# Optimization experiments

Measured on AMD Instinct MI355X. Metric: run time of the kernel, lower is better.

Reference implementation:

```python
import jax, jax.numpy as jnp
import numpy as np

B, L, E = 4, 2048, 768
H, MLP = 12, 3072
DH = E // H
N_HASHES, QC, KC = 4, 128, 128
EPS = 1e-6


def _layernorm(x, g, b):
    m = jnp.mean(x, -1, keepdims=True)
    v = jnp.mean((x - m) ** 2, -1, keepdims=True)
    return (x - m) * jax.lax.rsqrt(v + EPS) * g + b


def _smyrf_attn(q, k, v, alpha, beta):
    # q, k, v: (bs, L, dh) with bs = B*H; q is pre-scaled by dh**-0.5
    bs, sl, dh = q.shape
    # ---- LSH clustering (no-grad region, matches torch.no_grad in SMYRF) ----
    qd = jax.lax.stop_gradient(q)
    kd = jax.lax.stop_gradient(k)
    q_sq = jnp.sum(qd * qd, -1, keepdims=True)
    k_sq = jnp.sum(kd * kd, -1, keepdims=True)
    m_tot = jnp.max(q_sq) + jnp.max(k_sq)  # XBOX+ max-norm constant
    zq = jnp.zeros_like(q_sq)
    Qx = jnp.concatenate([qd, jnp.sqrt(jnp.maximum(m_tot - q_sq, 0.0)), zq], -1)
    Kx = jnp.concatenate([kd, zq, jnp.sqrt(jnp.maximum(m_tot - k_sq, 0.0))], -1)
    # E2LSH: scalar projection per hash round; sort positions by hash value
    q_pos = jnp.argsort(jnp.transpose(Qx @ alpha + beta, (2, 0, 1)), -1)  # (nh, bs, L)
    k_pos = jnp.argsort(jnp.transpose(Kx @ alpha + beta, (2, 0, 1)), -1)

    def gather(x, pos):  # (bs,L,d), (nh,bs,L) -> (nh,bs,L,d)
        xb = jnp.broadcast_to(x[None], (N_HASHES,) + x.shape)
        return jnp.take_along_axis(xb, pos[..., None], axis=2)

    s_q = gather(q, q_pos).reshape(N_HASHES, bs, sl // QC, QC, dh)
    s_k = gather(k, k_pos).reshape(N_HASHES, bs, sl // KC, KC, dh)
    s_v = gather(v, k_pos).reshape(N_HASHES, bs, sl // KC, KC, dh)

    # within-cluster attention
    inner = jnp.einsum('hbnqd,hbnkd->hbnqk', s_q, s_k)
    lse = jax.nn.logsumexp(inner, axis=-1, keepdims=True)
    bo = jnp.einsum('hbnqk,hbnkd->hbnqd', jnp.exp(inner - lse), s_v)
    bo = bo.reshape(N_HASHES, bs, sl, dh)

    # undo the sort, merge hash rounds weighted by softmax denominators
    q_rev = jnp.argsort(q_pos, -1)  # (nh, bs, L)
    o = jnp.take_along_axis(bo, q_rev[..., None], axis=2)
    logits = jnp.take_along_axis(lse.reshape(N_HASHES, bs, sl), q_rev, axis=2)
    probs = jnp.exp(logits - jax.nn.logsumexp(logits, axis=0, keepdims=True))
    return jnp.sum(o * probs[..., None], axis=0)  # (bs, L, dh)


def reference(x, ln1_g, ln1_b, w_qkv, b_qkv, w_out, b_out, ln2_g, ln2_b,
              w1, b1, w2, b2, alpha, beta):
    h = _layernorm(x, ln1_g, ln1_b)
    qkv = h @ w_qkv.T + b_qkv  # (B, L, 3E)
    q, k, v = jnp.split(qkv, 3, axis=-1)
    to_heads = lambda t: t.reshape(B, L, H, DH).transpose(0, 2, 1, 3).reshape(B * H, L, DH)
    attn = _smyrf_attn(to_heads(q) * (DH ** -0.5), to_heads(k), to_heads(v), alpha, beta)
    attn = attn.reshape(B, H, L, DH).transpose(0, 2, 1, 3).reshape(B, L, E)
    x2 = x + attn @ w_out.T + b_out  # residual (dropout is identity at rate 0)
    y = _layernorm(x2, ln2_g, ln2_b)
    y = jax.nn.gelu(y @ w1.T + b1, approximate=False) @ w2.T + b2
    return x2 + y


def setup_inputs() -> dict:
    key = jax.random.key(0)
    ks = jax.random.split(key, 8)
    s = 0.02
    return {
        'x': jax.random.normal(ks[0], (B, L, E), jnp.float32),
        'ln1_g': jnp.ones((E,), jnp.float32),
        'ln1_b': jnp.zeros((E,), jnp.float32),
        'w_qkv': jax.random.normal(ks[1], (3 * E, E), jnp.float32) * s,
        'b_qkv': jnp.zeros((3 * E,), jnp.float32),
        'w_out': jax.random.normal(ks[2], (E, E), jnp.float32) * s,
        'b_out': jnp.zeros((E,), jnp.float32),
        'ln2_g': jnp.ones((E,), jnp.float32),
        'ln2_b': jnp.zeros((E,), jnp.float32),
        'w1': jax.random.normal(ks[3], (MLP, E), jnp.float32) * s,
        'b1': jnp.zeros((MLP,), jnp.float32),
        'w2': jax.random.normal(ks[4], (E, MLP), jnp.float32) * s,
        'b2': jnp.zeros((E,), jnp.float32),
        'alpha': jax.random.normal(ks[5], (DH + 2, N_HASHES), jnp.float32),
        'beta': jax.random.uniform(ks[6], (N_HASHES,), jnp.float32),
    }
```

## Files before the change

### kernel.cpp

```cpp
#include <hip/hip_runtime.h>
#include <hip/hip_bf16.h>

#define NB 4
#define SL 2048
#define EM 768
#define NHD 12
#define DHD 64
#define MLPD 3072
#define NHASH 4
#define NBS 48
#define NPOS 98304
#define MLROWS 8192

typedef __attribute__((ext_vector_type(8))) short short8;
typedef __attribute__((ext_vector_type(8))) _Float16 f16x8;
typedef __attribute__((ext_vector_type(4))) float f32x4;

__device__ __forceinline__ unsigned short f2bf(float x){
  unsigned u = __float_as_uint(x);
  u += 0x7fffu + ((u>>16)&1u);
  return (unsigned short)(u>>16);
}
__device__ __forceinline__ float bf2f(unsigned short s){
  return __uint_as_float(((unsigned)s)<<16);
}
__device__ __forceinline__ int sw128(int row, int colbyte){ return row*128 + (colbyte ^ ((row&7)<<4)); }
__device__ __forceinline__ int sw256(int row, int colbyte){ return row*256 + (colbyte ^ ((row&7)<<4)); }
__device__ __forceinline__ int sw64(int row, int slot){ return row*64 + ((slot ^ ((row>>1)&3))<<4); }

__device__ __forceinline__ void gll16(const void* g, const void* l){
  __builtin_amdgcn_global_load_lds(
      (const __attribute__((address_space(1))) void*)(uintptr_t)g,
      (__attribute__((address_space(3))) void*)(unsigned int)(uintptr_t)l,
      16, 0, 0);
}

__global__ __launch_bounds__(256) void prep_all(const float* __restrict__ wqkv,
    const float* __restrict__ wout, const float* __restrict__ w1, const float* __restrict__ w2,
    const float* __restrict__ bqkv, const float* __restrict__ alpha,
    const float* __restrict__ x, const float* __restrict__ ln1g, const float* __restrict__ ln1b,
    _Float16* __restrict__ wq_h, _Float16* __restrict__ wq_l,
    unsigned short* __restrict__ wo_b, unsigned short* __restrict__ w1_b, unsigned short* __restrict__ w2_b,
    _Float16* __restrict__ wh_h, _Float16* __restrict__ wh_l, float* __restrict__ bias_h,
    _Float16* __restrict__ hh, _Float16* __restrict__ hl){
  int bid = blockIdx.x, tid = threadIdx.x;
  if (bid < 27648){
    int i = bid*256 + tid;
    if (i < 1769472){
      float v = wqkv[i]*1024.0f;
      _Float16 h = (_Float16)v;
      wq_h[i] = h;
      wq_l[i] = (_Float16)((v - (float)h)*2048.0f);
    } else if (i < 2359296){
      int j = i - 1769472; wo_b[j] = f2bf(wout[j]);
    } else if (i < 4718592){
      int j = i - 2359296; w1_b[j] = f2bf(w1[j]);
    } else {
      int j = i - 4718592; w2_b[j] = f2bf(w2[j]);
    }
    return;
  }
  if (bid < 27776){
    int row = bid - 27648;
    if (row >= 96){
      for (int c = tid; c < 768; c += 256){ wh_h[row*768+c] = (_Float16)0.f; wh_l[row*768+c] = (_Float16)0.f; }
      if (tid==0) bias_h[row] = 0.f;
      return;
    }
    int qk = row/48, hh2 = (row%48)>>2, r = row&3;
    float s = qk ? 1.0f : 0.125f;
    int base = qk*768 + hh2*64;
    for (int c = tid; c < 768; c += 256){
      float acc = 0.f;
      #pragma unroll 8
      for (int d=0; d<64; d++)
        acc += wqkv[(size_t)(base+d)*768 + c] * alpha[d*4 + r];
      float v = acc*s*1024.0f;
      _Float16 h = (_Float16)v;
      wh_h[row*768+c] = h;
      wh_l[row*768+c] = (_Float16)((v - (float)h)*2048.0f);
    }
    if (tid==0){
      float b = 0.f;
      for (int d=0; d<64; d++) b += bqkv[base+d]*alpha[d*4+r];
      bias_h[row] = b*s;
    }
    return;
  }
  int row = bid - 27776;
  __shared__ float sb[8];
  const float* xr = x + (size_t)row*EM;
  float v0 = xr[tid], v1 = xr[tid+256], v2 = xr[tid+512];
  float s = v0+v1+v2;
  #pragma unroll
  for (int off=32; off; off>>=1) s += __shfl_down(s, off);
  if ((tid&63)==0) sb[tid>>6] = s;
  __syncthreads();
  float mean = (sb[0]+sb[1]+sb[2]+sb[3]) * (1.0f/768.0f);
  float d0=v0-mean, d1=v1-mean, d2=v2-mean;
  float q_ = d0*d0 + d1*d1 + d2*d2;
  #pragma unroll
  for (int off=32; off; off>>=1) q_ += __shfl_down(q_, off);
  __syncthreads();
  if ((tid&63)==0) sb[tid>>6] = q_;
  __syncthreads();
  float var = (sb[0]+sb[1]+sb[2]+sb[3]) * (1.0f/768.0f);
  float rs = rsqrtf(var + 1e-6f);
  float dv[3] = {d0,d1,d2};
  #pragma unroll
  for (int e=0;e<3;e++){
    int cc = tid + e*256;
    float val = dv[e]*rs*ln1g[cc] + ln1b[cc];
    size_t oi = (size_t)row*EM + cc;
    _Float16 h = (_Float16)val;
    hh[oi] = h;
    hl[oi] = (_Float16)((val - (float)h)*2048.0f);
  }
}

__global__ __launch_bounds__(256) void ln2_kernel(const unsigned short* __restrict__ xb,
    const float* __restrict__ g, const float* __restrict__ bb, unsigned short* __restrict__ ob){
  int row = blockIdx.x; int tid = threadIdx.x;
  __shared__ float sb[8];
  float v[4] = {0.f,0.f,0.f,0.f};
  const bool act = tid < 192;
  if (act){
    uint2 u = *(const uint2*)(xb + (size_t)row*EM + tid*4);
    v[0]=bf2f((unsigned short)(u.x&0xFFFF)); v[1]=bf2f((unsigned short)(u.x>>16));
    v[2]=bf2f((unsigned short)(u.y&0xFFFF)); v[3]=bf2f((unsigned short)(u.y>>16));
  }
  float s = v[0]+v[1]+v[2]+v[3];
  #pragma unroll
  for (int off=32; off; off>>=1) s += __shfl_down(s, off);
  if ((tid&63)==0) sb[tid>>6] = s;
  __syncthreads();
  float mean = (sb[0]+sb[1]+sb[2]+sb[3]) * (1.0f/768.0f);
  float d[4], q_ = 0.f;
  #pragma unroll
  for (int e=0;e<4;e++){ d[e] = act ? v[e]-mean : 0.f; q_ += d[e]*d[e]; }
  #pragma unroll
  for (int off=32; off; off>>=1) q_ += __shfl_down(q_, off);
  __syncthreads();
  if ((tid&63)==0) sb[tid>>6] = q_;
  __syncthreads();
  float var = (sb[0]+sb[1]+sb[2]+sb[3]) * (1.0f/768.0f);
  float rs = rsqrtf(var + 1e-6f);
  if (act){
    unsigned short o[4];
    #pragma unroll
    for (int e=0;e<4;e++){
      int cc = tid*4+e;
      o[e] = f2bf(d[e]*rs*g[cc] + bb[cc]);
    }
    uint2 u; u.x = (unsigned)o[0] | ((unsigned)o[1]<<16); u.y = (unsigned)o[2] | ((unsigned)o[3]<<16);
    *(uint2*)(ob + (size_t)row*EM + tid*4) = u;
  }
}

__global__ __launch_bounds__(512) void qkv_gemm(const _Float16* __restrict__ Ah, const _Float16* __restrict__ Al,
    const _Float16* __restrict__ Wh, const _Float16* __restrict__ Wl,
    const _Float16* __restrict__ wh_h, const _Float16* __restrict__ wh_l,
    const float* __restrict__ bias, const float* __restrict__ bias_h,
    unsigned short* __restrict__ qb16, unsigned short* __restrict__ kb16, unsigned short* __restrict__ vo,
    float* __restrict__ qsq, float* __restrict__ ksq, unsigned* __restrict__ scal,
    float* __restrict__ hqp, float* __restrict__ hkp){
  __shared__ __align__(16) char smem[65536];
  __shared__ float smx_s[8];
  const int tid=threadIdx.x, l=tid&63, w=tid>>6, wm=w>>1, wn=w&1;
  const int by = blockIdx.y;
  const int m0 = blockIdx.x*128;
  const int srow = l>>2;
  const int scol = ((l&3)^((l>>3)&3))<<3;
  int oa[2], ob_[4];
  #pragma unroll
  for (int i=0;i<2;i++) oa[i]  = sw64(wm*32 + i*16 + (l&15), l>>4);
  #pragma unroll
  for (int j=0;j<4;j++) ob_[j] = sw64(wn*64 + j*16 + (l&15), l>>4);
  const bool ishash = (by == 18);
  if (by < 12 || ishash){
    const int n0 = ishash ? 0 : by*128;
    const _Float16* Bh0 = ishash ? wh_h : (Wh + (size_t)n0*EM);
    const _Float16* Bl0 = ishash ? wh_l : (Wl + (size_t)n0*EM);
    const _Float16* pAh = Ah  + (size_t)(m0 + w*16 + srow)*EM + scol;
    const _Float16* pAl = Al  + (size_t)(m0 + w*16 + srow)*EM + scol;
    const _Float16* pBh = Bh0 + (size_t)(w*16 + srow)*EM + scol;
    const _Float16* pBl = Bl0 + (size_t)(w*16 + srow)*EM + scol;
    f32x4 a1[2][4] = {}; f32x4 a2[2][4] = {};
    auto stage = [&](int buf, int k0){
      char* b = smem + buf*32768 + w*1024;
      gll16(pAh + k0, b);
      gll16(pAl + k0, b +  8192);
      gll16(pBh + k0, b + 16384);
      gll16(pBl + k0, b + 24576);
    };
    auto compute = [&](int buf){
      char* s0 = smem + buf*32768;
      f16x8 ah[2], al2[2];
      #pragma unroll
      for (int i=0;i<2;i++){
        ah[i]  = *(const f16x8*)(s0 + oa[i]);
        al2[i] = *(const f16x8*)(s0 + 8192 + oa[i]);
      }
      #pragma unroll
      for (int j=0;j<4;j++){
        f16x8 bh = *(const f16x8*)(s0 + 16384 + ob_[j]);
        f16x8 bl = *(const f16x8*)(s0 + 24576 + ob_[j]);
        #pragma unroll
        for (int i=0;i<2;i++){
          a1[i][j] = __builtin_amdgcn_mfma_f32_16x16x32_f16(ah[i],  bh, a1[i][j],0,0,0);
          a2[i][j] = __builtin_amdgcn_mfma_f32_16x16x32_f16(ah[i],  bl, a2[i][j],0,0,0);
          a2[i][j] = __builtin_amdgcn_mfma_f32_16x16x32_f16(al2[i], bh, a2[i][j],0,0,0);
        }
      }
    };
    stage(0, 0);
    __syncthreads();
    #pragma unroll 2
    for (int t=0;t<24;t++){
      if (t<23) stage((t+1)&1, (t+1)*32);
      compute(t&1);
      __syncthreads();
    }
    if (ishash){
      #pragma unroll
      for (int i=0;i<2;i++)
      #pragma unroll
      for (int rr=0;rr<4;rr++){
        int gm = m0 + wm*32 + i*16 + (l>>4)*4 + rr;
        int b = gm>>11, ll = gm&2047;
        #pragma unroll
        for (int j=0;j<4;j++){
          int col = wn*64 + j*16 + (l&15);
          if (col < 96){
            float v = (a1[i][j][rr] + a2[i][j][rr]*4.8828125e-4f)*9.765625e-4f + bias_h[col];
            int qk = col/48, hh = (col%48)>>2, r = col&3;
            size_t pos = ((size_t)(b*NHD+hh))*SL + ll;
            (qk ? hkp : hqp)[(size_t)r*NPOS + pos] = v;
          }
        }
      }
    } else {
      const bool isq = (by < 6);
      const float so = isq ? 0.125f : 1.0f;
      unsigned short* ob16 = isq ? qb16 : kb16;
      float* sqout = isq ? qsq : ksq;
      const int gn0 = n0 + wn*64;
      const int hh = (isq ? gn0 : gn0-768)>>6;
      float mx = 0.f;
      #pragma unroll
      for (int i=0;i<2;i++)
      #pragma unroll
      for (int rr=0;rr<4;rr++){
        int gm = m0 + wm*32 + i*16 + (l>>4)*4 + rr;
        int b = gm>>11, ll = gm&2047;
        size_t pos = ((size_t)(b*NHD+hh))*SL + ll;
        float vv[4]; float sq_p = 0.f;
        #pragma unroll
        for (int j=0;j<4;j++){
          int gn = gn0 + j*16 + (l&15);
          float v = (a1[i][j][rr] + a2[i][j][rr]*4.8828125e-4f)*9.765625e-4f + bias[gn];
          v *= so;
          vv[j] = v;
          sq_p += v*v;
        }
        #pragma unroll
        for (int j=0;j<4;j++)
          ob16[pos*DHD + j*16 + (l&15)] = f2bf(vv[j]);
        #pragma unroll
        for (int off2=1; off2<16; off2<<=1) sq_p += __shfl_xor(sq_p, off2);
        mx = fmaxf(mx, sq_p);
        if ((l&15)==0) sqout[pos] = sq_p;
      }
      mx = fmaxf(mx, __shfl_xor(mx, 16));
      mx = fmaxf(mx, __shfl_xor(mx, 32));
      if (l==0) smx_s[w] = mx;
      __syncthreads();
      if (tid==0){
        float m2 = smx_s[0];
        #pragma unroll
        for (int q2=1;q2<8;q2++) m2 = fmaxf(m2, smx_s[q2]);
        atomicMax(scal + (isq?0:1), __float_as_uint(m2));
      }
    }
  } else {
    const int n0 = (by-12)*128;
    const _Float16* pAh = Ah + (size_t)(m0 + w*16 + srow)*EM + scol;
    const _Float16* pBh = Wh + (size_t)(1536 + n0 + w*16 + srow)*EM + scol;
    f32x4 acc[2][4] = {};
    auto stage = [&](int buf, int k0){
      char* b = smem + buf*16384 + w*1024;
      gll16(pAh + k0, b);
      gll16(pBh + k0, b + 8192);
    };
    auto compute = [&](int buf){
      char* s0 = smem + buf*16384;
      f16x8 ah[2];
      #pragma unroll
      for (int i=0;i<2;i++) ah[i] = *(const f16x8*)(s0 + oa[i]);
      #pragma unroll
      for (int j=0;j<4;j++){
        f16x8 bh = *(const f16x8*)(s0 + 8192 + ob_[j]);
        #pragma unroll
        for (int i=0;i<2;i++)
          acc[i][j] = __builtin_amdgcn_mfma_f32_16x16x32_f16(ah[i], bh, acc[i][j],0,0,0);
      }
    };
    stage(0, 0);
    __syncthreads();
    #pragma unroll 2
    for (int t=0;t<24;t++){
      if (t<23) stage((t+1)&1, (t+1)*32);
      compute(t&1);
      __syncthreads();
    }
    #pragma unroll
    for (int i=0;i<2;i++)
    #pragma unroll
    for (int j=0;j<4;j++)
    #pragma unroll
    for (int rr=0;rr<4;rr++){
      int gm = m0 + wm*32 + i*16 + (l>>4)*4 + rr;
      int gn = n0 + wn*64 + j*16 + (l&15);
      float v = acc[i][j][rr]*9.765625e-4f + bias[1536+gn];
      int hh = gn>>6; int d = gn&63;
      int b = gm>>11; int ll = gm&2047;
      vo[(((size_t)(b*NHD+hh))*SL + ll)*DHD + d] = f2bf(v);
    }
  }
}

__global__ __launch_bounds__(1024) void sort_kernel(const float* __restrict__ hqp, const float* __restrict__ hkp,
    const float* __restrict__ qsq, const float* __restrict__ ksq, const unsigned* __restrict__ scal,
    const float* __restrict__ alpha, const float* __restrict__ beta,
    int* __restrict__ qpos, int* __restrict__ kpos){
  __shared__ unsigned long long sv[2048];
  int bid = blockIdx.x;
  bool isq = bid < 192;
  int row = isq ? bid : bid-192;
  int r = row/NBS, bs = row%NBS;
  const float* hp  = (isq?hqp:hkp) + (size_t)r*NPOS + (size_t)bs*SL;
  const float* sqp = (isq?qsq:ksq) + (size_t)bs*SL;
  int* op = (isq?qpos:kpos) + (size_t)row*SL;
  float m_tot = __uint_as_float(scal[0]) + __uint_as_float(scal[1]);
  float ae = alpha[(isq?64:65)*4 + r];
  float be = beta[r];
  const int wv = threadIdx.x>>6, lane = threadIdx.x&63, seg = wv*128;
  #pragma unroll
  for (int s=0; s<2; s++){
    int i = seg + s*64 + lane;
    float ext = sqrtf(fmaxf(m_tot - sqp[i], 0.f));
    float h = hp[i] + ext*ae + be;
    unsigned u = __float_as_uint(h);
    u ^= ((unsigned)((int)u>>31)) | 0x80000000u;
    sv[i] = ((unsigned long long)u<<32) | (unsigned)i;
  }
  for (int kk=2; kk<=SL; kk<<=1){
    for (int j=kk>>1; j>0; j>>=1){
      if (j >= 64 && kk >= 256) __syncthreads();
      int t = threadIdx.x;
      int i1 = ((t & ~(j-1))<<1) | (t & (j-1));
      int i2 = i1 | j;
      bool up = (i1 & kk)==0;
      unsigned long long a = sv[i1], b = sv[i2];
      if ((a>b)==up){ sv[i1]=b; sv[i2]=a; }
    }
  }
  #pragma unroll
  for (int s=0; s<2; s++){
    int i = seg + s*64 + lane;
    op[i] = (int)(unsigned)(sv[i] & 0xFFFFFFFFu);
  }
}

__global__ __launch_bounds__(256) void attn_kernel(const unsigned short* __restrict__ qb,
    const unsigned short* __restrict__ kb, const unsigned short* __restrict__ v,
    const int* __restrict__ qpos, const int* __restrict__ kpos,
    unsigned short* __restrict__ oh, float* __restrict__ lseh){
  __shared__ __align__(16) char smem[50176];
  char* qs  = smem;
  char* ks_ = smem + 16384;
  char* P   = smem;
  char* vt  = smem + 32768;
  int* idxq = (int*)(smem + 49152);
  int* idxk = (int*)(smem + 49664);

  const int tid = threadIdx.x, l = tid&63, w = tid>>6;
  const int lg = (((int)blockIdx.x)&7)*384 + (((int)blockIdx.x)>>3);
  const int c = lg&15, r = (lg>>4)&3, bs = lg>>6;
  const size_t rowbase = ((size_t)r*NBS + bs)*SL;
  if (tid < 128) idxq[tid] = qpos[rowbase + c*128 + tid];
  else           idxk[tid-128] = kpos[rowbase + c*128 + (tid-128)];
  __syncthreads();

  const unsigned short* qbb = qb + (size_t)bs*SL*DHD;
  const unsigned short* kbb = kb + (size_t)bs*SL*DHD;
  const unsigned short* vb  = v  + (size_t)bs*SL*DHD;
  #pragma unroll
  for (int p=0;p<4;p++){
    int row = p*32 + (tid>>3); int ch = tid&7;
    {
      int orig = idxq[row];
      uint4 u = *(const uint4*)(qbb + (size_t)orig*DHD + ch*8);
      *(uint4*)(qs + sw128(row, ch*16)) = u;
    }
    {
      int orig = idxk[row];
      uint4 u = *(const uint4*)(kbb + (size_t)orig*DHD + ch*8);
      *(uint4*)(ks_ + sw128(row, ch*16)) = u;
    }
    {
      int orig = idxk[row];
      uint4 vv = *(const uint4*)(vb + (size_t)orig*DHD + ch*8);
      unsigned short arr[8];
      *(uint4*)arr = vv;
      #pragma unroll
      for (int ii=0;ii<8;ii++){
        int d = ch*8+ii;
        *(unsigned short*)(vt + sw256(d, row*2)) = arr[ii];
      }
    }
  }
  __syncthreads();

  f32x4 sc[2][8] = {};
  __builtin_amdgcn_s_setprio(1);
  #pragma unroll
  for (int ks=0;ks<2;ks++){
    int cb = ks*64 + ((l>>4)<<4);
    short8 aq[2];
    aq[0] = *(const short8*)(qs + sw128(w*32 +      (l&15), cb));
    aq[1] = *(const short8*)(qs + sw128(w*32 + 16 + (l&15), cb));
    #pragma unroll
    for (int nj=0;nj<8;nj++){
      short8 bk = *(const short8*)(ks_ + sw128(nj*16+(l&15), cb));
      sc[0][nj] = __builtin_amdgcn_mfma_f32_16x16x32_bf16(aq[0], bk, sc[0][nj],0,0,0);
      sc[1][nj] = __builtin_amdgcn_mfma_f32_16x16x32_bf16(aq[1], bk, sc[1][nj],0,0,0);
    }
  }
  __builtin_amdgcn_s_setprio(0);
  __syncthreads();

  #pragma unroll
  for (int mi=0;mi<2;mi++)
  #pragma unroll
  for (int rr=0;rr<4;rr++){
    float mx = -3.0e38f;
    #pragma unroll
    for (int nj=0;nj<8;nj++) mx = fmaxf(mx, sc[mi][nj][rr]);
    #pragma unroll
    for (int off=1; off<16; off<<=1) mx = fmaxf(mx, __shfl_xor(mx, off));
    float s = 0.f;
    #pragma unroll
    for (int nj=0;nj<8;nj++){ float p_ = expf(sc[mi][nj][rr]-mx); sc[mi][nj][rr]=p_; s += p_; }
    #pragma unroll
    for (int off=1; off<16; off<<=1) s += __shfl_xor(s, off);
    float inv = 1.0f/s;
    int row = w*32 + mi*16 + (l>>4)*4 + rr;
    #pragma unroll
    for (int nj=0;nj<8;nj++){
      int col = nj*16 + (l&15);
      *(unsigned short*)(P + sw256(row, col*2)) = f2bf(sc[mi][nj][rr]*inv);
    }
    if ((l&15)==0){
      int orig = idxq[row];
      lseh[rowbase + orig] = mx + logf(s);
    }
  }
  __syncthreads();

  f32x4 o[2][4] = {};
  __builtin_amdgcn_s_setprio(1);
  #pragma unroll
  for (int ks=0;ks<4;ks++){
    int cb = ks*64 + ((l>>4)<<4);
    short8 pa[2];
    pa[0] = *(const short8*)(P + sw256(w*32 +      (l&15), cb));
    pa[1] = *(const short8*)(P + sw256(w*32 + 16 + (l&15), cb));
    #pragma unroll
    for (int nd=0;nd<4;nd++){
      short8 bv = *(const short8*)(vt + sw256(nd*16+(l&15), cb));
      o[0][nd] = __builtin_amdgcn_mfma_f32_16x16x32_bf16(pa[0], bv, o[0][nd],0,0,0);
      o[1][nd] = __builtin_amdgcn_mfma_f32_16x16x32_bf16(pa[1], bv, o[1][nd],0,0,0);
    }
  }
  __builtin_amdgcn_s_setprio(0);
  #pragma unroll
  for (int mi=0;mi<2;mi++)
  #pragma unroll
  for (int nd=0;nd<4;nd++)
  #pragma unroll
  for (int rr=0;rr<4;rr++){
    int row = w*32 + mi*16 + (l>>4)*4 + rr;
    int orig = idxq[row];
    oh[(rowbase + orig)*DHD + nd*16 + (l&15)] = f2bf(o[mi][nd][rr]);
  }
}

__global__ __launch_bounds__(256) void merge_kernel(const unsigned short* __restrict__ oh,
    const float* __restrict__ lseh, unsigned short* __restrict__ attnb){
  int g = blockIdx.x*256 + threadIdx.x;
  int pos = g>>4; int d0 = (g&15)<<2;
  int ll = pos & (SL-1); int bs = pos >> 11;
  float l0 = lseh[0*NPOS+pos], l1 = lseh[1*NPOS+pos], l2 = lseh[2*NPOS+pos], l3 = lseh[3*NPOS+pos];
  float mx = fmaxf(fmaxf(l0,l1),fmaxf(l2,l3));
  float w0 = expf(l0-mx), w1 = expf(l1-mx), w2 = expf(l2-mx), w3 = expf(l3-mx);
  float inv = 1.0f/(w0+w1+w2+w3);
  w0 *= inv; w1 *= inv; w2 *= inv; w3 *= inv;
  uint2 u0 = *(const uint2*)(oh + ((size_t)0*NPOS+pos)*DHD + d0);
  uint2 u1 = *(const uint2*)(oh + ((size_t)1*NPOS+pos)*DHD + d0);
  uint2 u2 = *(const uint2*)(oh + ((size_t)2*NPOS+pos)*DHD + d0);
  uint2 u3 = *(const uint2*)(oh + ((size_t)3*NPOS+pos)*DHD + d0);
  unsigned short a0[4], a1[4], a2[4], a3[4], ro[4];
  *(uint2*)a0 = u0; *(uint2*)a1 = u1; *(uint2*)a2 = u2; *(uint2*)a3 = u3;
  #pragma unroll
  for (int e=0;e<4;e++){
    float acc = w0*bf2f(a0[e]) + w1*bf2f(a1[e]) + w2*bf2f(a2[e]) + w3*bf2f(a3[e]);
    ro[e] = f2bf(acc);
  }
  int b = bs/NHD, hh = bs%NHD;
  *(uint2*)(attnb + ((size_t)(b*SL)+ll)*EM + hh*DHD + d0) = *(uint2*)ro;
}

template<int EPI, int BN>
__global__ __launch_bounds__(512) void gemm_bf16(const unsigned short* __restrict__ A,
    const unsigned short* __restrict__ Bw, const float* __restrict__ bias,
    const float* __restrict__ res_f, const unsigned short* __restrict__ res_b,
    float* __restrict__ outf, unsigned short* __restrict__ outb,
    int M, int N, int K){
  constexpr int NJ = BN/32;
  constexpr int BB = BN*64;
  constexpr int BUF = 8192 + BB;
  __shared__ __align__(16) char smem[2*BUF];
  const int tid=threadIdx.x, l=tid&63, w=tid>>6, wm=w>>1, wn=w&1;
  const int m0 = blockIdx.x*128, n0 = blockIdx.y*BN;
  const int srow = l>>2, scol = ((l&3)^((l>>3)&3))<<3;
  f32x4 acc[2][NJ] = {};
  const unsigned short* pA = A  + (size_t)(m0 + w*16 + srow)*K + scol;
  const unsigned short* pB = Bw + (size_t)(n0 + w*16 + srow)*K + scol;
  int oa[2], ob_[NJ];
  #pragma unroll
  for (int i=0;i<2;i++)  oa[i]  = sw64(wm*32 + i*16 + (l&15), l>>4);
  #pragma unroll
  for (int j=0;j<NJ;j++) ob_[j] = sw64(wn*(BN/2) + j*16 + (l&15), l>>4);
  auto stage = [&](int buf, int k0){
    char* bA = smem + buf*BUF;
    char* bB = bA + 8192;
    gll16(pA + k0, bA + w*1024);
    if (BN==128 || w < 4)
      gll16(pB + k0, bB + w*1024);
  };
  auto compute = [&](int buf){
    char* bA = smem + buf*BUF;
    char* bB = bA + 8192;
    short8 af[2], bfr[NJ];
    #pragma unroll
    for (int i=0;i<2;i++)  af[i]  = *(const short8*)(bA + oa[i]);
    #pragma unroll
    for (int j=0;j<NJ;j++) bfr[j] = *(const short8*)(bB + ob_[j]);
    #pragma unroll
    for (int i=0;i<2;i++)
    #pragma unroll
    for (int j=0;j<NJ;j++)
      acc[i][j] = __builtin_amdgcn_mfma_f32_16x16x32_bf16(af[i], bfr[j], acc[i][j],0,0,0);
  };
  const int nt = K/32;
  stage(0, 0);
  __syncthreads();
  #pragma unroll 2
  for (int t=0;t<nt;t++){
    if (t<nt-1) stage((t+1)&1, (t+1)*32);
    compute(t&1);
    __syncthreads();
  }
  #pragma unroll
  for (int i=0;i<2;i++)
  #pragma unroll
  for (int j=0;j<NJ;j++)
  #pragma unroll
  for (int rr=0;rr<4;rr++){
    int gm = m0 + wm*32 + i*16 + (l>>4)*4 + rr;
    int gn = n0 + wn*(BN/2) + j*16 + (l&15);
    float v = acc[i][j][rr] + bias[gn];
    size_t oidx = (size_t)gm*N + gn;
    if (EPI==1){ float ge = 0.5f*v*(1.0f + erff(v*0.70710678118654752f)); outb[oidx] = f2bf(ge); }
    else if (EPI==2){ outb[oidx] = f2bf(v + res_f[oidx]); }
    else { outf[oidx] = v + bf2f(res_b[oidx]); }
  }
}

extern "C" void kernel_launch(void* const* d_in, const int* in_sizes, int n_in,
                              void* d_out, int out_size, void* d_ws, size_t ws_size,
                              hipStream_t stream){
  const float* x    = (const float*)d_in[0];
  const float* ln1g = (const float*)d_in[1];
  const float* ln1b = (const float*)d_in[2];
  const float* wqkv = (const float*)d_in[3];
  const float* bqkv = (const float*)d_in[4];
  const float* wout = (const float*)d_in[5];
  const float* bout = (const float*)d_in[6];
  const float* ln2g = (const float*)d_in[7];
  const float* ln2b = (const float*)d_in[8];
  const float* w1   = (const float*)d_in[9];
  const float* b1   = (const float*)d_in[10];
  const float* w2   = (const float*)d_in[11];
  const float* b2   = (const float*)d_in[12];
  const float* alpha= (const float*)d_in[13];
  const float* beta = (const float*)d_in[14];
  float* out = (float*)d_out;

  char* ws = (char*)d_ws;
  size_t off = 0;
  auto A = [&](size_t n)->char*{ char* p = ws+off; off += (n+255)&~(size_t)255; return p; };
  _Float16* h_hi = (_Float16*)A(12582912);
  _Float16* h_lo = (_Float16*)A(12582912);
  _Float16* wq_h = (_Float16*)A(3538944);
  _Float16* wq_l = (_Float16*)A(3538944);
  unsigned short* wo_b = (unsigned short*)A(1179648);
  unsigned short* w1_b = (unsigned short*)A(4718592);
  unsigned short* w2_b = (unsigned short*)A(4718592);
  _Float16* wh_h = (_Float16*)A(196608);
  _Float16* wh_l = (_Float16*)A(196608);
  float* bias_h  = (float*)A(512);
  unsigned short* qb16 = (unsigned short*)A(12582912);
  unsigned short* kb16 = (unsigned short*)A(12582912);
  unsigned short* vbuf = (unsigned short*)A(12582912);
  float* qsq = (float*)A(393216);
  float* ksq = (float*)A(393216);
  unsigned* scal = (unsigned*)A(256);
  float* hqp = (float*)A(1572864);
  float* hkp = (float*)A(1572864);
  int* qpos = (int*)A(1572864);
  int* kpos = (int*)A(1572864);
  unsigned short* oh = (unsigned short*)A(50331648);
  float* lseh = (float*)A(1572864);
  unsigned short* ub = (unsigned short*)A(50331648);
  unsigned short* attnb = vbuf;
  unsigned short* x2b = (unsigned short*)oh;
  unsigned short* yb = (unsigned short*)h_hi;

  hipMemsetAsync(scal, 0, 8, stream);
  prep_all<<<35968, 256, 0, stream>>>(wqkv, wout, w1, w2, bqkv, alpha, x, ln1g, ln1b,
                                      wq_h, wq_l, wo_b, w1_b, w2_b, wh_h, wh_l, bias_h, h_hi, h_lo);
  qkv_gemm<<<dim3(64,19), 512, 0, stream>>>(h_hi, h_lo, wq_h, wq_l, wh_h, wh_l, bqkv, bias_h,
                                            qb16, kb16, vbuf, qsq, ksq, scal, hqp, hkp);
  sort_kernel<<<384, 1024, 0, stream>>>(hqp, hkp, qsq, ksq, scal, alpha, beta, qpos, kpos);
  attn_kernel<<<3072, 256, 0, stream>>>(qb16, kb16, vbuf, qpos, kpos, oh, lseh);
  merge_kernel<<<6144, 256, 0, stream>>>(oh, lseh, attnb);
  gemm_bf16<2,64><<<dim3(64,12),  512, 0, stream>>>(attnb, wo_b, bout, x, nullptr, nullptr, x2b, MLROWS, 768, 768);
  ln2_kernel<<<MLROWS, 256, 0, stream>>>(x2b, ln2g, ln2b, yb);
  gemm_bf16<1,128><<<dim3(64,24), 512, 0, stream>>>(yb, w1_b, b1, nullptr, nullptr, nullptr, ub, MLROWS, 3072, 768);
  gemm_bf16<3,64><<<dim3(64,12),  512, 0, stream>>>(ub, w2_b, b2, nullptr, x2b, out, nullptr, MLROWS, 768, 3072);
}
```

Baseline: 370.0 us.

## Replace double-buffered QKV GEMM staging with single-buffer load-sync-compute loop

Removes the double-buffered LDS pipeline in the QKV GEMM and uses a single 32KB buffer, with a barrier before and after each K-slice load. Halving shared memory per block could let more blocks reside per CU. In exchange the global-to-LDS loads no longer overlap with MFMA compute inside a block, and each iteration adds a second barrier.

```diff
diff --git a/kernel.cpp b/kernel.cpp
--- a/kernel.cpp
+++ b/kernel.cpp
@@ -164,7 +164,7 @@
     unsigned short* __restrict__ qb16, unsigned short* __restrict__ kb16, unsigned short* __restrict__ vo,
     float* __restrict__ qsq, float* __restrict__ ksq, unsigned* __restrict__ scal,
     float* __restrict__ hqp, float* __restrict__ hkp){
-  __shared__ __align__(16) char smem[65536];
+  __shared__ __align__(16) char smem[32768];
   __shared__ float smx_s[8];
   const int tid=threadIdx.x, l=tid&63, w=tid>>6, wm=w>>1, wn=w&1;
   const int by = blockIdx.y;
@@ -186,25 +186,27 @@
     const _Float16* pBh = Bh0 + (size_t)(w*16 + srow)*EM + scol;
     const _Float16* pBl = Bl0 + (size_t)(w*16 + srow)*EM + scol;
     f32x4 a1[2][4] = {}; f32x4 a2[2][4] = {};
-    auto stage = [&](int buf, int k0){
-      char* b = smem + buf*32768 + w*1024;
-      gll16(pAh + k0, b);
-      gll16(pAl + k0, b +  8192);
-      gll16(pBh + k0, b + 16384);
-      gll16(pBl + k0, b + 24576);
-    };
-    auto compute = [&](int buf){
-      char* s0 = smem + buf*32768;
+    for (int t=0;t<24;t++){
+      int k0 = t*32;
+      __syncthreads();
+      {
+        char* b = smem + w*1024;
+        gll16(pAh + k0, b);
+        gll16(pAl + k0, b +  8192);
+        gll16(pBh + k0, b + 16384);
+        gll16(pBl + k0, b + 24576);
+      }
+      __syncthreads();
       f16x8 ah[2], al2[2];
       #pragma unroll
       for (int i=0;i<2;i++){
-        ah[i]  = *(const f16x8*)(s0 + oa[i]);
-        al2[i] = *(const f16x8*)(s0 + 8192 + oa[i]);
+        ah[i]  = *(const f16x8*)(smem + oa[i]);
+        al2[i] = *(const f16x8*)(smem + 8192 + oa[i]);
       }
       #pragma unroll
       for (int j=0;j<4;j++){
-        f16x8 bh = *(const f16x8*)(s0 + 16384 + ob_[j]);
-        f16x8 bl = *(const f16x8*)(s0 + 24576 + ob_[j]);
+        f16x8 bh = *(const f16x8*)(smem + 16384 + ob_[j]);
+        f16x8 bl = *(const f16x8*)(smem + 24576 + ob_[j]);
         #pragma unroll
         for (int i=0;i<2;i++){
           a1[i][j] = __builtin_amdgcn_mfma_f32_16x16x32_f16(ah[i],  bh, a1[i][j],0,0,0);
@@ -212,14 +214,6 @@
           a2[i][j] = __builtin_amdgcn_mfma_f32_16x16x32_f16(al2[i], bh, a2[i][j],0,0,0);
         }
       }
-    };
-    stage(0, 0);
-    __syncthreads();
-    #pragma unroll 2
-    for (int t=0;t<24;t++){
-      if (t<23) stage((t+1)&1, (t+1)*32);
-      compute(t&1);
-      __syncthreads();
     }
     if (ishash){
       #pragma unroll
@@ -287,31 +281,25 @@
     const _Float16* pAh = Ah + (size_t)(m0 + w*16 + srow)*EM + scol;
     const _Float16* pBh = Wh + (size_t)(1536 + n0 + w*16 + srow)*EM + scol;
     f32x4 acc[2][4] = {};
-    auto stage = [&](int buf, int k0){
-      char* b = smem + buf*16384 + w*1024;
-      gll16(pAh + k0, b);
-      gll16(pBh + k0, b + 8192);
-    };
-    auto compute = [&](int buf){
-      char* s0 = smem + buf*16384;
+    for (int t=0;t<24;t++){
+      int k0 = t*32;
+      __syncthreads();
+      {
+        char* b = smem + w*1024;
+        gll16(pAh + k0, b);
+        gll16(pBh + k0, b + 8192);
+      }
+      __syncthreads();
       f16x8 ah[2];
       #pragma unroll
-      for (int i=0;i<2;i++) ah[i] = *(const f16x8*)(s0 + oa[i]);
+      for (int i=0;i<2;i++) ah[i] = *(const f16x8*)(smem + oa[i]);
       #pragma unroll
       for (int j=0;j<4;j++){
-        f16x8 bh = *(const f16x8*)(s0 + 8192 + ob_[j]);
+        f16x8 bh = *(const f16x8*)(smem + 8192 + ob_[j]);
         #pragma unroll
         for (int i=0;i<2;i++)
           acc[i][j] = __builtin_amdgcn_mfma_f32_16x16x32_f16(ah[i], bh, acc[i][j],0,0,0);
       }
-    };
-    stage(0, 0);
-    __syncthreads();
-    #pragma unroll 2
-    for (int t=0;t<24;t++){
-      if (t<23) stage((t+1)&1, (t+1)*32);
-      compute(t&1);
-      __syncthreads();
     }
     #pragma unroll
     for (int i=0;i<2;i++)
```

New measurement: 372.0 us. No clear change (+0.6%).

## Load Q fragments straight to registers and reuse K buffer for P in two halves

Applied to the files above, without the earlier changes.

The attention kernel now loads Q MFMA operands directly from global memory into registers via the gathered indices, so the Q shared-memory tile disappears. The probability matrix is written in two 64-column halves into the reused K buffer, so LDS per block drops from about 49KB to about 33KB and more blocks can reside per CU. The cost is more registers held across phases and an extra P write/MFMA round per half. Each wave touches only its own rows in the reused buffer, so the barrier before the PV phase is removed, which relies on per-wave row ownership.

```diff
diff --git a/kernel.cpp b/kernel.cpp
--- a/kernel.cpp
+++ b/kernel.cpp
@@ -376,13 +376,11 @@
     const unsigned short* __restrict__ kb, const unsigned short* __restrict__ v,
     const int* __restrict__ qpos, const int* __restrict__ kpos,
     unsigned short* __restrict__ oh, float* __restrict__ lseh){
-  __shared__ __align__(16) char smem[50176];
-  char* qs  = smem;
-  char* ks_ = smem + 16384;
-  char* P   = smem;
-  char* vt  = smem + 32768;
-  int* idxq = (int*)(smem + 49152);
-  int* idxk = (int*)(smem + 49664);
+  __shared__ __align__(16) char smem[33792];
+  char* ks_ = smem;
+  char* vt  = smem + 16384;
+  int* idxq = (int*)(smem + 32768);
+  int* idxk = (int*)(smem + 33280);
 
   const int tid = threadIdx.x, l = tid&63, w = tid>>6;
   const int lg = (((int)blockIdx.x)&7)*384 + (((int)blockIdx.x)>>3);
@@ -395,14 +393,18 @@
   const unsigned short* qbb = qb + (size_t)bs*SL*DHD;
   const unsigned short* kbb = kb + (size_t)bs*SL*DHD;
   const unsigned short* vb  = v  + (size_t)bs*SL*DHD;
+
+  short8 aq[2][2];
+  #pragma unroll
+  for (int mi=0;mi<2;mi++){
+    int orig = idxq[w*32 + mi*16 + (l&15)];
+    const unsigned short* qp = qbb + (size_t)orig*DHD + ((l>>4)<<3);
+    aq[mi][0] = *(const short8*)(qp);
+    aq[mi][1] = *(const short8*)(qp + 32);
+  }
   #pragma unroll
   for (int p=0;p<4;p++){
     int row = p*32 + (tid>>3); int ch = tid&7;
-    {
-      int orig = idxq[row];
-      uint4 u = *(const uint4*)(qbb + (size_t)orig*DHD + ch*8);
-      *(uint4*)(qs + sw128(row, ch*16)) = u;
-    }
     {
       int orig = idxk[row];
       uint4 u = *(const uint4*)(kbb + (size_t)orig*DHD + ch*8);
@@ -427,14 +429,11 @@
   #pragma unroll
   for (int ks=0;ks<2;ks++){
     int cb = ks*64 + ((l>>4)<<4);
-    short8 aq[2];
-    aq[0] = *(const short8*)(qs + sw128(w*32 +      (l&15), cb));
-    aq[1] = *(const short8*)(qs + sw128(w*32 + 16 + (l&15), cb));
     #pragma unroll
     for (int nj=0;nj<8;nj++){
       short8 bk = *(const short8*)(ks_ + sw128(nj*16+(l&15), cb));
-      sc[0][nj] = __builtin_amdgcn_mfma_f32_16x16x32_bf16(aq[0], bk, sc[0][nj],0,0,0);
-      sc[1][nj] = __builtin_amdgcn_mfma_f32_16x16x32_bf16(aq[1], bk, sc[1][nj],0,0,0);
+      sc[0][nj] = __builtin_amdgcn_mfma_f32_16x16x32_bf16(aq[0][ks], bk, sc[0][nj],0,0,0);
+      sc[1][nj] = __builtin_amdgcn_mfma_f32_16x16x32_bf16(aq[1][ks], bk, sc[1][nj],0,0,0);
     }
   }
   __builtin_amdgcn_s_setprio(0);
@@ -455,35 +454,45 @@
     #pragma unroll
     for (int off=1; off<16; off<<=1) s += __shfl_xor(s, off);
     float inv = 1.0f/s;
-    int row = w*32 + mi*16 + (l>>4)*4 + rr;
-    #pragma unroll
-    for (int nj=0;nj<8;nj++){
-      int col = nj*16 + (l&15);
-      *(unsigned short*)(P + sw256(row, col*2)) = f2bf(sc[mi][nj][rr]*inv);
-    }
+    #pragma unroll
+    for (int nj=0;nj<8;nj++) sc[mi][nj][rr] *= inv;
     if ((l&15)==0){
+      int row = w*32 + mi*16 + (l>>4)*4 + rr;
       int orig = idxq[row];
       lseh[rowbase + orig] = mx + logf(s);
     }
   }
-  __syncthreads();
 
   f32x4 o[2][4] = {};
-  __builtin_amdgcn_s_setprio(1);
-  #pragma unroll
-  for (int ks=0;ks<4;ks++){
-    int cb = ks*64 + ((l>>4)<<4);
-    short8 pa[2];
-    pa[0] = *(const short8*)(P + sw256(w*32 +      (l&15), cb));
-    pa[1] = *(const short8*)(P + sw256(w*32 + 16 + (l&15), cb));
-    #pragma unroll
-    for (int nd=0;nd<4;nd++){
-      short8 bv = *(const short8*)(vt + sw256(nd*16+(l&15), cb));
-      o[0][nd] = __builtin_amdgcn_mfma_f32_16x16x32_bf16(pa[0], bv, o[0][nd],0,0,0);
-      o[1][nd] = __builtin_amdgcn_mfma_f32_16x16x32_bf16(pa[1], bv, o[1][nd],0,0,0);
-    }
-  }
-  __builtin_amdgcn_s_setprio(0);
+  #pragma unroll
+  for (int half=0; half<2; half++){
+    #pragma unroll
+    for (int mi=0;mi<2;mi++)
+    #pragma unroll
+    for (int rr=0;rr<4;rr++){
+      int row = w*32 + mi*16 + (l>>4)*4 + rr;
+      #pragma unroll
+      for (int nj2=0;nj2<4;nj2++)
+        *(unsigned short*)(ks_ + sw128(row, (nj2*16 + (l&15))*2)) = f2bf(sc[mi][half*4+nj2][rr]);
+    }
+    __builtin_amdgcn_s_setprio(1);
+    #pragma unroll
+    for (int k2=0;k2<2;k2++){
+      int ksg = half*2 + k2;
+      int cb  = k2*64 + ((l>>4)<<4);
+      int cbv = ksg*64 + ((l>>4)<<4);
+      short8 pa[2];
+      pa[0] = *(const short8*)(ks_ + sw128(w*32 +      (l&15), cb));
+      pa[1] = *(const short8*)(ks_ + sw128(w*32 + 16 + (l&15), cb));
+      #pragma unroll
+      for (int nd=0;nd<4;nd++){
+        short8 bv = *(const short8*)(vt + sw256(nd*16+(l&15), cbv));
+        o[0][nd] = __builtin_amdgcn_mfma_f32_16x16x32_bf16(pa[0], bv, o[0][nd],0,0,0);
+        o[1][nd] = __builtin_amdgcn_mfma_f32_16x16x32_bf16(pa[1], bv, o[1][nd],0,0,0);
+      }
+    }
+    __builtin_amdgcn_s_setprio(0);
+  }
   #pragma unroll
   for (int mi=0;mi<2;mi++)
   #pragma unroll
```

After: 377.1 us. Within noise of the previous version (+1.9%).
